# Kernel optimization log

Measured on AMD Instinct MI355X. Metric: run time of the kernel, lower is better.

Reference implementation:

```python
import jax, jax.numpy as jnp
import numpy as np

jax.config.update("jax_enable_x64", True)  # FixedPointMul math is done in float64, as in torch

B, S, H = 8, 4096, 768


def setup_inputs():
    key = jax.random.key(0)
    k = jax.random.split(key, 6)
    s_act = jnp.array([4.0 / 127.0], dtype=jnp.float32)  # per-tensor 8-bit activation scale

    def qact(kk):  # produce int8-quantized-looking activations
        x = jax.random.normal(kk, (B, S, H), jnp.float32)
        return s_act * jnp.clip(jnp.round(x / s_act), -128, 127)

    return {
        "hidden_states": qact(k[0]),
        "hidden_states_scaling_factor": s_act,
        "input_tensor": qact(k[1]),
        "input_tensor_scaling_factor": s_act,
        "dense_weight": 0.02 * jax.random.normal(k[2], (H, H), jnp.float32),
        "dense_bias": 0.01 * jax.random.normal(k[3], (H,), jnp.float32),
        "ln_weight": 1.0 + 0.05 * jax.random.normal(k[4], (H,), jnp.float32),
        "ln_bias": 0.05 * jax.random.normal(k[5], (H,), jnp.float32),
    }


def _sym_scale(k, smin, smax):
    n = 2 ** (k - 1) - 1
    return jnp.clip(jnp.maximum(jnp.abs(smin), jnp.abs(smax)), 1e-8, None) / n


def _sym_quant(x, k, scale):
    n = 2 ** (k - 1) - 1
    return jnp.clip(jnp.round(x / scale), -n, n - 1)


def _batch_frexp(x):
    # returns (round(mantissa * 2^31), 31 - exponent) as in ibert batch_frexp
    m, e = jnp.frexp(x)
    return jnp.floor(m * (2.0 ** 31) + 0.5), 31.0 - e


def _fixedpoint_mul(x, pre_scale, bit, z_scale, identity=None, id_scale=None):
    n = 2 ** (bit - 1) - 1
    ps = jnp.reshape(pre_scale, (1, 1, -1)).astype(jnp.float64)
    z = z_scale.astype(jnp.float64)
    z_int = jnp.round(x.astype(jnp.float64) / ps)
    m, e = _batch_frexp(ps / z)
    out = jnp.round(z_int * m / (2.0 ** e))
    if identity is not None:
        isf = jnp.reshape(id_scale, (1, 1, -1)).astype(jnp.float64)
        wx = jnp.round(identity.astype(jnp.float64) / isf)
        m1, e1 = _batch_frexp(isf / z)
        out = out + jnp.round(wx * m1 / (2.0 ** e1))
    return jnp.clip(out, -n - 1, n).astype(jnp.float32)


def _quant_act(x, bit, pre_scale, identity=None, id_scale=None):
    x_act = x if identity is None else x + identity
    s = _sym_scale(bit, x_act.min(), x_act.max())  # per-tensor scale (dynamic range)
    q = _fixedpoint_mul(x, pre_scale, bit, s, identity, id_scale)
    return q * s, s


def reference(hidden_states, hidden_states_scaling_factor, input_tensor, input_tensor_scaling_factor, dense_weight, dense_bias, ln_weight, ln_bias):
    # ---- QuantLinear: per-channel int8 weights, int32 bias ----
    w_min = dense_weight.min(axis=1)
    w_max = dense_weight.max(axis=1)
    fc_scale = _sym_scale(8, w_min, w_max)                      # [H_out]
    w_int = _sym_quant(dense_weight, 8, fc_scale[:, None])      # [H_out, H_in]
    bias_scale = fc_scale * hidden_states_scaling_factor        # [H_out]
    b_int = _sym_quant(dense_bias, 32, bias_scale)
    x_int = hidden_states / hidden_states_scaling_factor
    hs = (jnp.einsum("bsh,oh->bso", x_int, w_int) + b_int) * bias_scale
    # dropout: eval mode -> identity
    # ---- QuantAct(22-bit) with quantized residual add ----
    hs, ln_in_scale = _quant_act(hs, 22, bias_scale, input_tensor, input_tensor_scaling_factor)
    # ---- IntLayerNorm (integer-only LayerNorm) ----
    x_int = hs / ln_in_scale
    mean_int = jnp.round(jnp.mean(x_int, axis=2, keepdims=True))
    y_int = x_int - mean_int
    var0 = jnp.sum(y_int ** 2, axis=2, keepdims=True)
    shift = jnp.ceil(jnp.log2(jnp.sqrt(jnp.maximum(var0, 1.0) / 2.0 ** 32)))  # set_shift (max_bit=32)
    shift = jnp.maximum(0.0, shift.max())
    y_sh = jnp.floor(y_int / 2.0 ** shift)
    var_int = jnp.sum(y_sh ** 2, axis=2, keepdims=True)
    std_int = jnp.floor(jnp.sqrt(var_int)) * 2.0 ** shift
    factor = jnp.floor(2.0 ** 31 / std_int)
    y_int = jnp.floor(y_int * factor / 2.0)
    sf = jnp.sqrt(jnp.float32(H)) / 2.0 ** 30
    bias_int = jnp.floor((ln_bias / ln_weight) / sf)
    y_int = y_int + bias_int
    sf_out = sf * ln_weight                                     # [H]
    hs = y_int * sf_out
    # ---- QuantAct(8-bit) output requantization ----
    hs, out_scale = _quant_act(hs, 8, sf_out)
    return hs, out_scale
```

## Files before the change

kernel.cpp:

```cpp
#include <hip/hip_runtime.h>

typedef int   v4i   __attribute__((ext_vector_type(4)));
typedef unsigned long u64x2 __attribute__((ext_vector_type(2)));

#define HDIM 768
#define NTOK 32768
#define NCAND 12

static constexpr size_t WX_OFF   = 0;
static constexpr size_t WINT_OFF = 25165824;
static constexpr size_t RS1_OFF  = WINT_OFF + 1179648;
static constexpr size_t RS2_OFF  = RS1_OFF + 6144;
static constexpr size_t BS_OFF   = RS2_OFF + 6144;
static constexpr size_t BINT_OFF = BS_OFF + 3072;
static constexpr size_t LNBI_OFF = BINT_OFF + 3072;
static constexpr size_t SFO_OFF  = LNBI_OFF + 3072;
static constexpr size_t SC_OFF   = SFO_OFF + 3072;
static constexpr size_t RSM1_OFF = SC_OFF + 64;
static constexpr size_t CMIN_OFF = SC_OFF + 128;
static constexpr size_t CMAX_OFF = SC_OFF + 192;
static constexpr size_t FCT_OFF  = SC_OFF + 256;

__device__ __forceinline__ unsigned fenc(float f) {
    unsigned u = __float_as_uint(f);
    return (u >> 31) ? ~u : (u | 0x80000000u);
}
__device__ __forceinline__ float fdec(unsigned e) {
    unsigned u = (e >> 31) ? (e & 0x7fffffffu) : ~e;
    return __uint_as_float(u);
}

#define GLDS16(g, l) __builtin_amdgcn_global_load_lds( \
    (const __attribute__((address_space(1))) unsigned int*)(g), \
    (__attribute__((address_space(3))) unsigned int*)(l), 16, 0, 0)

__device__ __forceinline__ int swz4(int r) { return (r & 3) ^ ((r >> 2) & 3); }

__global__ __launch_bounds__(256) void k0_prep(const float* __restrict__ W,
                                               const float* __restrict__ bias,
                                               const float* __restrict__ ln_w,
                                               const float* __restrict__ ln_b,
                                               const float* __restrict__ phsf,
                                               char* __restrict__ ws) {
    int o = blockIdx.x, tid = threadIdx.x;
    __shared__ float red[256];
    __shared__ float fc_sh;
    float m = 0.f;
    for (int j = tid; j < HDIM; j += 256) m = fmaxf(m, fabsf(W[(size_t)o * HDIM + j]));
    red[tid] = m;
    __syncthreads();
    for (int s = 128; s; s >>= 1) { if (tid < s) red[tid] = fmaxf(red[tid], red[tid + s]); __syncthreads(); }
    if (tid == 0) {
        float fc = fmaxf(red[0], 1e-8f) / 127.0f;
        float hsf = *phsf;
        float bs = fc * hsf;
        fc_sh = fc;
        ((float*)(ws + BS_OFF))[o] = bs;
        ((int*)(ws + BINT_OFF))[o] = (int)rintf(bias[o] / bs);
        float sf = sqrtf(768.0f) / 1073741824.0f;
        float lw = ln_w[o], lb = ln_b[o];
        ((int*)(ws + LNBI_OFF))[o] = (int)floorf((lb / lw) / sf);
        ((float*)(ws + SFO_OFF))[o] = sf * lw;
    }
    __syncthreads();
    float fc = fc_sh;
    char* w8 = (char*)(ws + WINT_OFF);
    for (int j = tid; j < HDIM; j += 256) {
        float q = rintf(W[(size_t)o * HDIM + j] / fc);
        q = fminf(fmaxf(q, -127.f), 126.f);
        w8[(size_t)o * HDIM + j] = (char)q;
    }
    if (blockIdx.x == 0) {
        if (tid < 8) {
            unsigned* sc = (unsigned*)(ws + SC_OFF);
            unsigned v = 0u;
            if (tid == 0 || tid == 2) v = 0xFFFFFFFFu;
            sc[tid] = v;
        }
        if (tid < 16) {
            ((unsigned*)(ws + CMIN_OFF))[tid] = 0xFFFFFFFFu;
            ((unsigned*)(ws + CMAX_OFF))[tid] = 0u;
        }
    }
}

__global__ __launch_bounds__(256) void kp_a8(const float* __restrict__ hs,
                                             const float* __restrict__ phsf,
                                             char* __restrict__ ws) {
    int tid = threadIdx.x;
    size_t b4 = (size_t)blockIdx.x * 1024 + tid;
    float inv = 1.0f / *phsf;
    const float4* in4 = (const float4*)hs;
    unsigned* o32 = (unsigned*)(ws + WX_OFF);
    #pragma unroll
    for (int j = 0; j < 4; ++j) {
        float4 v = in4[b4 + j * 256];
        int q0 = (int)rintf(v.x * inv), q1 = (int)rintf(v.y * inv);
        int q2 = (int)rintf(v.z * inv), q3 = (int)rintf(v.w * inv);
        o32[b4 + j * 256] = (unsigned)(q0 & 255) | ((unsigned)(q1 & 255) << 8) |
                            ((unsigned)(q2 & 255) << 16) | ((unsigned)(q3 & 255) << 24);
    }
}

#define BM 128
#define BN 128
#define BK 64
#define NKT (HDIM / BK)
#define SROW 132
__global__ __launch_bounds__(256, 3) void k1_gemm(const float* __restrict__ inp,
                                                  char* __restrict__ ws,
                                                  int* __restrict__ accOut) {
    __shared__ alignas(16) char smem[32800];
    char* As0 = smem;
    char* Bs0 = smem + 16384;
    float* rmn = (float*)(smem + 32768);
    float* rmx = rmn + 4;
    int tid = threadIdx.x, lane = tid & 63, wave = tid >> 6;
    int wrow = lane & 15, g = lane >> 4;
    int bid = blockIdx.x;
    int xcd = bid & 7, slot = bid >> 3;
    int mtile = xcd * 32 + slot / 6;
    int ntile = slot % 6;
    int t0 = mtile * BM, o0 = ntile * BN;
    const char* a8 = (const char*)(ws + WX_OFF);
    const char* w8 = (const char*)(ws + WINT_OFF);

    const char* asrc[2]; const char* bsrc[2];
    int ldso[2];
    #pragma unroll
    for (int i = 0; i < 2; ++i) {
        int c = i * 256 + tid, r = c >> 2, s = c & 3;
        asrc[i] = a8 + (size_t)(t0 + r) * HDIM + (s ^ swz4(r)) * 16;
        bsrc[i] = w8 + (size_t)(o0 + r) * HDIM + (s ^ swz4(r)) * 16;
        ldso[i] = (i * 256 + wave * 64) * 16;
    }

    int wm = wave & 1, wn = wave >> 1;
    int aofs[4], bofs[4];
    #pragma unroll
    for (int mi = 0; mi < 4; ++mi) { int r = wm * 64 + mi * 16 + wrow; aofs[mi] = r * BK + ((g ^ swz4(r)) * 16); }
    #pragma unroll
    for (int nf = 0; nf < 4; ++nf) { int r = wn * 64 + nf * 16 + wrow; bofs[nf] = r * BK + ((g ^ swz4(r)) * 16); }

    #pragma unroll
    for (int i = 0; i < 2; ++i) GLDS16(asrc[i], As0 + ldso[i]);
    #pragma unroll
    for (int i = 0; i < 2; ++i) GLDS16(bsrc[i], Bs0 + ldso[i]);
    #pragma unroll
    for (int i = 0; i < 2; ++i) GLDS16(asrc[i] + BK, As0 + 8192 + ldso[i]);
    #pragma unroll
    for (int i = 0; i < 2; ++i) GLDS16(bsrc[i] + BK, Bs0 + 8192 + ldso[i]);
    asm volatile("s_waitcnt vmcnt(4)" ::: "memory");
    __builtin_amdgcn_s_barrier();

    v4i acc[4][4] = {};
    for (int kt = 0; kt < NKT; ++kt) {
        int cur = kt & 1;
        const char* Ac = As0 + cur * 8192;
        const char* Bc = Bs0 + cur * 8192;
        u64x2 af[4], bf[4];
        #pragma unroll
        for (int mi = 0; mi < 4; ++mi) af[mi] = *(const u64x2*)(Ac + aofs[mi]);
        #pragma unroll
        for (int nf = 0; nf < 4; ++nf) bf[nf] = *(const u64x2*)(Bc + bofs[nf]);
        asm volatile("s_waitcnt lgkmcnt(0)" ::: "memory");
        __builtin_amdgcn_s_barrier();
        if (kt + 2 < NKT) {
            #pragma unroll
            for (int i = 0; i < 2; ++i) GLDS16(asrc[i] + (kt + 2) * BK, As0 + cur * 8192 + ldso[i]);
            #pragma unroll
            for (int i = 0; i < 2; ++i) GLDS16(bsrc[i] + (kt + 2) * BK, Bs0 + cur * 8192 + ldso[i]);
        }
        __builtin_amdgcn_s_setprio(1);
        #pragma unroll
        for (int mi = 0; mi < 4; ++mi)
            #pragma unroll
            for (int nf = 0; nf < 4; ++nf) {
                acc[mi][nf] = __builtin_amdgcn_mfma_i32_16x16x32_i8((long)af[mi][0], (long)bf[nf][0], acc[mi][nf], 0, 0, 0);
                acc[mi][nf] = __builtin_amdgcn_mfma_i32_16x16x32_i8((long)af[mi][1], (long)bf[nf][1], acc[mi][nf], 0, 0, 0);
            }
        __builtin_amdgcn_s_setprio(0);
        if (kt + 2 < NKT) {
            asm volatile("s_waitcnt vmcnt(4)" ::: "memory");
            __builtin_amdgcn_s_barrier();
        } else if (kt + 2 == NKT) {
            asm volatile("s_waitcnt vmcnt(0)" ::: "memory");
            __builtin_amdgcn_s_barrier();
        }
    }

    const float* bscale = (const float*)(ws + BS_OFF);
    const int* bint = (const int*)(ws + BINT_OFF);
    int* sAcc = (int*)smem;
    float lmn = 3.402823466e38f, lmx = -3.402823466e38f;
    #pragma unroll
    for (int mi = 0; mi < 4; ++mi) {
        __syncthreads();
        #pragma unroll
        for (int nf = 0; nf < 4; ++nf)
            #pragma unroll
            for (int r = 0; r < 4; ++r)
                sAcc[(wm * 16 + g * 4 + r) * SROW + wn * 64 + nf * 16 + wrow] = acc[mi][nf][r];
        __syncthreads();
        #pragma unroll
        for (int k = 0; k < 4; ++k) {
            int i4 = tid + k * 256;
            int sr = i4 >> 5, c4 = i4 & 31;
            int t = t0 + (sr >> 4) * 64 + mi * 16 + (sr & 15);
            int col = o0 + c4 * 4;
            int4 a4 = *(const int4*)&sAcc[sr * SROW + c4 * 4];
            int4 b4 = *(const int4*)&bint[col];
            float4 bs4 = *(const float4*)&bscale[col];
            a4.x += b4.x; a4.y += b4.y; a4.z += b4.z; a4.w += b4.w;
            size_t idx = (size_t)t * HDIM + col;
            *(int4*)&accOut[idx] = a4;
            float4 x4 = *(const float4*)&inp[idx];
            float xa;
            xa = (float)a4.x * bs4.x + x4.x; lmn = fminf(lmn, xa); lmx = fmaxf(lmx, xa);
            xa = (float)a4.y * bs4.y + x4.y; lmn = fminf(lmn, xa); lmx = fmaxf(lmx, xa);
            xa = (float)a4.z * bs4.z + x4.z; lmn = fminf(lmn, xa); lmx = fmaxf(lmx, xa);
            xa = (float)a4.w * bs4.w + x4.w; lmn = fminf(lmn, xa); lmx = fmaxf(lmx, xa);
        }
    }
    #pragma unroll
    for (int off = 32; off; off >>= 1) {
        lmn = fminf(lmn, __shfl_down(lmn, off));
        lmx = fmaxf(lmx, __shfl_down(lmx, off));
    }
    __syncthreads();
    if (lane == 0) { rmn[wave] = lmn; rmx[wave] = lmx; }
    __syncthreads();
    if (tid == 0) {
        float mn = fminf(fminf(rmn[0], rmn[1]), fminf(rmn[2], rmn[3]));
        float mx = fmaxf(fmaxf(rmx[0], rmx[1]), fmaxf(rmx[2], rmx[3]));
        volatile unsigned* sc = (volatile unsigned*)(ws + SC_OFF);
        unsigned emn = fenc(mn), emx = fenc(mx);
        if (emn < sc[0]) atomicMin((unsigned*)&sc[0], emn);
        if (emx > sc[1]) atomicMax((unsigned*)&sc[1], emx);
    }
}

__global__ __launch_bounds__(256) void k2_scale1(const float* __restrict__ pisf, char* __restrict__ ws) {
    __shared__ float s_sh;
    unsigned* sc = (unsigned*)(ws + SC_OFF);
    if (threadIdx.x == 0) {
        float mn = fdec(sc[0]), mx = fdec(sc[1]);
        float s = fmaxf(fmaxf(fabsf(mn), fabsf(mx)), 1e-8f) / 2097151.0f;
        ((float*)sc)[5] = s;
        s_sh = s;
        double r = (double)(*pisf) / (double)s;
        int ex; double mant = frexp(r, &ex);
        double m1 = floor(mant * 2147483648.0 + 0.5);
        ((double*)(ws + RSM1_OFF))[0] = m1 * exp2((double)(ex - 31));
    }
    __syncthreads();
    float s = s_sh;
    const float* bs = (const float*)(ws + BS_OFF);
    double* rs1 = (double*)(ws + RS1_OFF);
    for (int o = threadIdx.x; o < HDIM; o += 256) {
        double r = (double)bs[o] / (double)s;
        int ex; double mant = frexp(r, &ex);
        double m = floor(mant * 2147483648.0 + 0.5);
        rs1[o] = m * exp2((double)(ex - 31));
    }
}

__global__ __launch_bounds__(256) void k3f(char* __restrict__ ws, int* __restrict__ buf,
                                           const float* __restrict__ inp,
                                           const float* __restrict__ pisf) {
    int tid = threadIdx.x, lane = tid & 63, wave = tid >> 6;
    int wid = blockIdx.x * 4 + wave;
    const double* rs1 = (const double*)(ws + RS1_OFF);
    double rsm1 = *(const double*)(ws + RSM1_OFF);
    float inv_isf = 1.0f / *pisf;
    const int* lnbi = (const int*)(ws + LNBI_OFF);
    const float* sfo = (const float*)(ws + SFO_OFF);
    unsigned* fct = (unsigned*)(ws + FCT_OFF);
    __shared__ float smn[4][NCAND], smx[4][NCAND];
    double t_rs1[12]; int t_lnbi[12]; float t_sfo[12];
    #pragma unroll
    for (int c = 0; c < 3; ++c) {
        int o0 = (lane + 64 * c) * 4;
        #pragma unroll
        for (int j = 0; j < 4; ++j) {
            t_rs1[c * 4 + j] = rs1[o0 + j];
            t_lnbi[c * 4 + j] = lnbi[o0 + j];
            t_sfo[c * 4 + j] = sfo[o0 + j];
        }
    }
    int localShift = 0;
    float cmn[NCAND], cmx[NCAND];
    #pragma unroll
    for (int s = 0; s < NCAND; ++s) { cmn[s] = 3.402823466e38f; cmx[s] = -3.402823466e38f; }
    int4 aP[3]; float4 xP[3];
    {
        size_t b0 = (size_t)(wid * 4) * HDIM;
        #pragma unroll
        for (int c = 0; c < 3; ++c) {
            aP[c] = ((const int4*)(buf + b0))[lane + 64 * c];
            xP[c] = ((const float4*)(inp + b0))[lane + 64 * c];
        }
    }
    for (int rr = 0; rr < 4; ++rr) {
        int4 aN[3]; float4 xN[3];
        if (rr < 3) {
            size_t nb = (size_t)(wid * 4 + rr + 1) * HDIM;
            #pragma unroll
            for (int c = 0; c < 3; ++c) {
                aN[c] = ((const int4*)(buf + nb))[lane + 64 * c];
                xN[c] = ((const float4*)(inp + nb))[lane + 64 * c];
            }
        }
        size_t base = (size_t)(wid * 4 + rr) * HDIM;
        int q[12];
        int sum = 0;
        #pragma unroll
        for (int c = 0; c < 3; ++c) {
            int av[4] = {aP[c].x, aP[c].y, aP[c].z, aP[c].w};
            float xv[4] = {xP[c].x, xP[c].y, xP[c].z, xP[c].w};
            #pragma unroll
            for (int j = 0; j < 4; ++j) {
                double q1 = rint((double)av[j] * t_rs1[c * 4 + j]);
                int wxj = (int)rintf(xv[j] * inv_isf);
                double qq = q1 + rint((double)wxj * rsm1);
                qq = fmin(fmax(qq, -2097152.0), 2097151.0);
                q[c * 4 + j] = (int)qq;
                sum += q[c * 4 + j];
            }
        }
        #pragma unroll
        for (int off = 32; off; off >>= 1) sum += __shfl_xor(sum, off);
        int mean = (int)rint((double)sum / 768.0);
        long long v0 = 0;
        #pragma unroll
        for (int k = 0; k < 12; ++k) { q[k] -= mean; v0 += (long long)q[k] * (long long)q[k]; }
        #pragma unroll
        for (int off = 32; off; off >>= 1) v0 += __shfl_xor(v0, off);
        #pragma unroll
        for (int c = 0; c < 3; ++c) {
            int4 y = {q[c * 4 + 0], q[c * 4 + 1], q[c * 4 + 2], q[c * 4 + 3]};
            ((int4*)(buf + base))[lane + 64 * c] = y;
        }
        double vd = (double)(v0 < 1 ? 1LL : v0);
        int sr = (int)ceil(0.5 * log2(vd) - 16.0);
        if (sr < 0) sr = 0;
        localShift = max(localShift, sr);
        #pragma unroll
        for (int s = 0; s < NCAND; ++s) {
            if (s >= sr) {
                long long vs;
                if (s == 0) vs = v0;
                else {
                    vs = 0;
                    #pragma unroll
                    for (int k = 0; k < 12; ++k) { int t = q[k] >> s; vs += (long long)t * (long long)t; }
                    #pragma unroll
                    for (int off = 32; off; off >>= 1) vs += __shfl_xor(vs, off);
                }
                double std_int = floor(sqrt((double)vs)) * (double)(1 << s);
                if (std_int < 1.0) std_int = 1.0;
                long long factor = (long long)floor(2147483648.0 / std_int);
                if (lane == 0) fct[(size_t)(wid * 4 + rr) * 16 + s] = (unsigned)factor;
                #pragma unroll
                for (int k = 0; k < 12; ++k) {
                    long long t = ((long long)q[k] * factor) >> 1;
                    int v2 = (int)t + t_lnbi[k];
                    float h = (float)v2 * t_sfo[k];
                    cmn[s] = fminf(cmn[s], h);
                    cmx[s] = fmaxf(cmx[s], h);
                }
            }
        }
        #pragma unroll
        for (int c = 0; c < 3; ++c) { aP[c] = aN[c]; xP[c] = xN[c]; }
    }
    if (lane == 0 && localShift > 0) {
        int* sp = (int*)(ws + SC_OFF) + 4;
        if (localShift > *(volatile int*)sp) atomicMax(sp, localShift);
    }
    #pragma unroll
    for (int s = 0; s < NCAND; ++s) {
        #pragma unroll
        for (int off = 32; off; off >>= 1) {
            cmn[s] = fminf(cmn[s], __shfl_xor(cmn[s], off));
            cmx[s] = fmaxf(cmx[s], __shfl_xor(cmx[s], off));
        }
    }
    if (lane == 0) {
        #pragma unroll
        for (int s = 0; s < NCAND; ++s) { smn[wave][s] = cmn[s]; smx[wave][s] = cmx[s]; }
    }
    __syncthreads();
    if (tid < NCAND) {
        float m = fminf(fminf(smn[0][tid], smn[1][tid]), fminf(smn[2][tid], smn[3][tid]));
        if (m < 3.3e38f) {
            volatile unsigned* cm = (volatile unsigned*)(ws + CMIN_OFF);
            unsigned e = fenc(m);
            if (e < cm[tid]) atomicMin((unsigned*)&cm[tid], e);
        }
    } else if (tid >= 64 && tid < 64 + NCAND) {
        int s = tid - 64;
        float m = fmaxf(fmaxf(smx[0][s], smx[1][s]), fmaxf(smx[2][s], smx[3][s]));
        if (m > -3.3e38f) {
            volatile unsigned* cm = (volatile unsigned*)(ws + CMAX_OFF);
            unsigned e = fenc(m);
            if (e > cm[s]) atomicMax((unsigned*)&cm[s], e);
        }
    }
}

__global__ __launch_bounds__(256) void k5_scale2(char* __restrict__ ws) {
    __shared__ float s_sh;
    if (threadIdx.x == 0) {
        int shift = ((const int*)(ws + SC_OFF))[4];
        float mn = fdec(((const unsigned*)(ws + CMIN_OFF))[shift]);
        float mx = fdec(((const unsigned*)(ws + CMAX_OFF))[shift]);
        float s2 = fmaxf(fmaxf(fabsf(mn), fabsf(mx)), 1e-8f) / 127.0f;
        ((float*)(ws + SC_OFF))[6] = s2;
        s_sh = s2;
    }
    __syncthreads();
    float s2 = s_sh;
    const float* sfo = (const float*)(ws + SFO_OFF);
    double* rs2 = (double*)(ws + RS2_OFF);
    for (int o = threadIdx.x; o < HDIM; o += 256) {
        double r = (double)sfo[o] / (double)s2;
        int ex; double mant = frexp(r, &ex);
        double m = floor(mant * 2147483648.0 + 0.5);
        rs2[o] = m * exp2((double)(ex - 31));
    }
}

__global__ __launch_bounds__(256) void k6_out(char* __restrict__ ws, float* __restrict__ out) {
    int tid = threadIdx.x, lane = tid & 63, wave = tid >> 6;
    int wid = blockIdx.x * 4 + wave;
    const double* rs2 = (const double*)(ws + RS2_OFF);
    const int* lnbi = (const int*)(ws + LNBI_OFF);
    const unsigned* fct = (const unsigned*)(ws + FCT_OFF);
    int shift = ((const int*)(ws + SC_OFF))[4];
    float s2 = ((const float*)(ws + SC_OFF))[6];
    double t_rs2[12]; int t_lnbi[12];
    #pragma unroll
    for (int c = 0; c < 3; ++c) {
        int o0 = (lane + 64 * c) * 4;
        #pragma unroll
        for (int j = 0; j < 4; ++j) { t_rs2[c * 4 + j] = rs2[o0 + j]; t_lnbi[c * 4 + j] = lnbi[o0 + j]; }
    }
    int* buf = (int*)out;
    int4 yP[3];
    {
        size_t b0 = (size_t)(wid * 4) * HDIM;
        #pragma unroll
        for (int c = 0; c < 3; ++c) yP[c] = ((const int4*)(buf + b0))[lane + 64 * c];
    }
    for (int rr = 0; rr < 4; ++rr) {
        int4 yN[3];
        if (rr < 3) {
            size_t nb = (size_t)(wid * 4 + rr + 1) * HDIM;
            #pragma unroll
            for (int c = 0; c < 3; ++c) yN[c] = ((const int4*)(buf + nb))[lane + 64 * c];
        }
        size_t base = (size_t)(wid * 4 + rr) * HDIM;
        long long factor = (long long)fct[(size_t)(wid * 4 + rr) * 16 + shift];
        int yv[12];
        #pragma unroll
        for (int c = 0; c < 3; ++c) {
            yv[c * 4 + 0] = yP[c].x; yv[c * 4 + 1] = yP[c].y; yv[c * 4 + 2] = yP[c].z; yv[c * 4 + 3] = yP[c].w;
        }
        #pragma unroll
        for (int c = 0; c < 3; ++c) {
            float4 r;
            float* rp = &r.x;
            #pragma unroll
            for (int j = 0; j < 4; ++j) {
                int k = c * 4 + j;
                long long t = ((long long)yv[k] * factor) >> 1;
                int v2 = (int)t + t_lnbi[k];
                double q = rint((double)v2 * t_rs2[k]);
                q = fmin(fmax(q, -128.0), 127.0);
                rp[j] = (float)q * s2;
            }
            ((float4*)(out + base))[lane + 64 * c] = r;
        }
        #pragma unroll
        for (int c = 0; c < 3; ++c) yP[c] = yN[c];
    }
    if (wid == 0 && tid == 0) out[(size_t)NTOK * HDIM] = s2;
}

extern "C" void kernel_launch(void* const* d_in, const int* in_sizes, int n_in,
                              void* d_out, int out_size, void* d_ws, size_t ws_size,
                              hipStream_t stream) {
    const float* hs   = (const float*)d_in[0];
    const float* phsf = (const float*)d_in[1];
    const float* inp  = (const float*)d_in[2];
    const float* pisf = (const float*)d_in[3];
    const float* W    = (const float*)d_in[4];
    const float* bias = (const float*)d_in[5];
    const float* ln_w = (const float*)d_in[6];
    const float* ln_b = (const float*)d_in[7];
    char* ws = (char*)d_ws;
    float* out = (float*)d_out;
    int* buf = (int*)d_out;

    k0_prep<<<HDIM, 256, 0, stream>>>(W, bias, ln_w, ln_b, phsf, ws);
    kp_a8<<<NTOK * HDIM / 4096, 256, 0, stream>>>(hs, phsf, ws);
    k1_gemm<<<(NTOK / BM) * (HDIM / BN), 256, 0, stream>>>(inp, ws, buf);
    k2_scale1<<<1, 256, 0, stream>>>(pisf, ws);
    k3f<<<NTOK / 16, 256, 0, stream>>>(ws, buf, inp, pisf);
    k5_scale2<<<1, 256, 0, stream>>>(ws);
    k6_out<<<NTOK / 16, 256, 0, stream>>>(ws, out);
}
```

Baseline: 422.9 us.

## Limit speculative LayerNorm shift candidates to four per row with fallback pass

The fused LayerNorm stage previously computed min/max statistics for every possible global shift from the row's own shift up to 11, to avoid a second pass. It now evaluates only four candidate shifts per row (sr..sr+3), reusing progressively shifted values, and tracks the minimum row shift. A flag kernel detects when the global shift lies outside that window, and a fallback kernel then recomputes the statistics from the stored centered values. This cuts per-row variance reductions and min/max work, at the cost of two extra launches and per-wave global atomics in place of block-level shared-memory aggregation.

```diff
diff --git a/kernel.cpp b/kernel.cpp
--- a/kernel.cpp
+++ b/kernel.cpp
@@ -5,7 +5,6 @@
 
 #define HDIM 768
 #define NTOK 32768
-#define NCAND 12
 
 static constexpr size_t WX_OFF   = 0;
 static constexpr size_t WINT_OFF = 25165824;
@@ -71,15 +70,16 @@
         w8[(size_t)o * HDIM + j] = (char)q;
     }
     if (blockIdx.x == 0) {
-        if (tid < 8) {
+        if (tid < 16) {
             unsigned* sc = (unsigned*)(ws + SC_OFF);
             unsigned v = 0u;
             if (tid == 0 || tid == 2) v = 0xFFFFFFFFu;
+            if (tid == 8) v = 127u;
             sc[tid] = v;
         }
-        if (tid < 16) {
-            ((unsigned*)(ws + CMIN_OFF))[tid] = 0xFFFFFFFFu;
-            ((unsigned*)(ws + CMAX_OFF))[tid] = 0u;
+        if (tid >= 32 && tid < 48) {
+            ((unsigned*)(ws + CMIN_OFF))[tid - 32] = 0xFFFFFFFFu;
+            ((unsigned*)(ws + CMAX_OFF))[tid - 32] = 0u;
         }
     }
 }
@@ -276,7 +276,8 @@
     const int* lnbi = (const int*)(ws + LNBI_OFF);
     const float* sfo = (const float*)(ws + SFO_OFF);
     unsigned* fct = (unsigned*)(ws + FCT_OFF);
-    __shared__ float smn[4][NCAND], smx[4][NCAND];
+    volatile unsigned* cmi = (volatile unsigned*)(ws + CMIN_OFF);
+    volatile unsigned* cma = (volatile unsigned*)(ws + CMAX_OFF);
     double t_rs1[12]; int t_lnbi[12]; float t_sfo[12];
     #pragma unroll
     for (int c = 0; c < 3; ++c) {
@@ -288,10 +289,7 @@
             t_sfo[c * 4 + j] = sfo[o0 + j];
         }
     }
-    int localShift = 0;
-    float cmn[NCAND], cmx[NCAND];
-    #pragma unroll
-    for (int s = 0; s < NCAND; ++s) { cmn[s] = 3.402823466e38f; cmx[s] = -3.402823466e38f; }
+    int locMax = 0, locMin = 127;
     int4 aP[3]; float4 xP[3];
     {
         size_t b0 = (size_t)(wid * 4) * HDIM;
@@ -344,16 +342,22 @@
         double vd = (double)(v0 < 1 ? 1LL : v0);
         int sr = (int)ceil(0.5 * log2(vd) - 16.0);
         if (sr < 0) sr = 0;
-        localShift = max(localShift, sr);
-        #pragma unroll
-        for (int s = 0; s < NCAND; ++s) {
-            if (s >= sr) {
+        if (sr > 11) sr = 11;
+        locMax = max(locMax, sr);
+        locMin = min(locMin, sr);
+        int z[12];
+        #pragma unroll
+        for (int k = 0; k < 12; ++k) z[k] = q[k] >> sr;
+        #pragma unroll
+        for (int d = 0; d < 4; ++d) {
+            int s = sr + d;
+            if (s < 12) {
                 long long vs;
-                if (s == 0) vs = v0;
+                if (d == 0 && sr == 0) vs = v0;
                 else {
                     vs = 0;
                     #pragma unroll
-                    for (int k = 0; k < 12; ++k) { int t = q[k] >> s; vs += (long long)t * (long long)t; }
+                    for (int k = 0; k < 12; ++k) vs += (long long)z[k] * (long long)z[k];
                     #pragma unroll
                     for (int off = 32; off; off >>= 1) vs += __shfl_xor(vs, off);
                 }
@@ -361,50 +365,101 @@
                 if (std_int < 1.0) std_int = 1.0;
                 long long factor = (long long)floor(2147483648.0 / std_int);
                 if (lane == 0) fct[(size_t)(wid * 4 + rr) * 16 + s] = (unsigned)factor;
+                float hmn = 3.402823466e38f, hmx = -3.402823466e38f;
                 #pragma unroll
                 for (int k = 0; k < 12; ++k) {
                     long long t = ((long long)q[k] * factor) >> 1;
                     int v2 = (int)t + t_lnbi[k];
                     float h = (float)v2 * t_sfo[k];
-                    cmn[s] = fminf(cmn[s], h);
-                    cmx[s] = fmaxf(cmx[s], h);
+                    hmn = fminf(hmn, h);
+                    hmx = fmaxf(hmx, h);
+                }
+                #pragma unroll
+                for (int off = 32; off; off >>= 1) {
+                    hmn = fminf(hmn, __shfl_xor(hmn, off));
+                    hmx = fmaxf(hmx, __shfl_xor(hmx, off));
+                }
+                if (lane == 0) {
+                    unsigned e = fenc(hmn);
+                    if (e < cmi[s]) atomicMin((unsigned*)&cmi[s], e);
+                    e = fenc(hmx);
+                    if (e > cma[s]) atomicMax((unsigned*)&cma[s], e);
                 }
             }
+            #pragma unroll
+            for (int k = 0; k < 12; ++k) z[k] >>= 1;
         }
         #pragma unroll
         for (int c = 0; c < 3; ++c) { aP[c] = aN[c]; xP[c] = xN[c]; }
     }
-    if (lane == 0 && localShift > 0) {
-        int* sp = (int*)(ws + SC_OFF) + 4;
-        if (localShift > *(volatile int*)sp) atomicMax(sp, localShift);
-    }
-    #pragma unroll
-    for (int s = 0; s < NCAND; ++s) {
+    if (lane == 0) {
+        int* sc = (int*)(ws + SC_OFF);
+        if (locMax > 0 && locMax > *(volatile int*)(sc + 4)) atomicMax(sc + 4, locMax);
+        if (locMin < *(volatile int*)(sc + 8)) atomicMin(sc + 8, locMin);
+    }
+}
+
+__global__ void k5a_flag(char* __restrict__ ws) {
+    if (threadIdx.x == 0) {
+        int S = ((const int*)(ws + SC_OFF))[4];
+        int smin = ((const int*)(ws + SC_OFF))[8];
+        ((int*)(ws + SC_OFF))[9] = (S - smin > 3) ? 1 : 0;
+    }
+}
+
+__global__ __launch_bounds__(256) void k4_fb(char* __restrict__ ws, const int* __restrict__ buf) {
+    if (*((volatile int*)(ws + SC_OFF) + 9) == 0) return;
+    int tid = threadIdx.x, lane = tid & 63, wave = tid >> 6;
+    int wid = blockIdx.x * 4 + wave;
+    int S = ((const int*)(ws + SC_OFF))[4];
+    const int* lnbi = (const int*)(ws + LNBI_OFF);
+    const float* sfo = (const float*)(ws + SFO_OFF);
+    unsigned* fct = (unsigned*)(ws + FCT_OFF);
+    volatile unsigned* cmi = (volatile unsigned*)(ws + CMIN_OFF);
+    volatile unsigned* cma = (volatile unsigned*)(ws + CMAX_OFF);
+    int t_lnbi[12]; float t_sfo[12];
+    #pragma unroll
+    for (int c = 0; c < 3; ++c) {
+        int o0 = (lane + 64 * c) * 4;
+        #pragma unroll
+        for (int j = 0; j < 4; ++j) { t_lnbi[c * 4 + j] = lnbi[o0 + j]; t_sfo[c * 4 + j] = sfo[o0 + j]; }
+    }
+    for (int rr = 0; rr < 4; ++rr) {
+        size_t base = (size_t)(wid * 4 + rr) * HDIM;
+        int yv[12];
+        #pragma unroll
+        for (int c = 0; c < 3; ++c) {
+            int4 y4 = ((const int4*)(buf + base))[lane + 64 * c];
+            yv[c * 4 + 0] = y4.x; yv[c * 4 + 1] = y4.y; yv[c * 4 + 2] = y4.z; yv[c * 4 + 3] = y4.w;
+        }
+        long long vs = 0;
+        #pragma unroll
+        for (int k = 0; k < 12; ++k) { int zz = yv[k] >> S; vs += (long long)zz * (long long)zz; }
+        #pragma unroll
+        for (int off = 32; off; off >>= 1) vs += __shfl_xor(vs, off);
+        double std_int = floor(sqrt((double)vs)) * (double)(1 << S);
+        if (std_int < 1.0) std_int = 1.0;
+        long long factor = (long long)floor(2147483648.0 / std_int);
+        if (lane == 0) fct[(size_t)(wid * 4 + rr) * 16 + S] = (unsigned)factor;
+        float hmn = 3.402823466e38f, hmx = -3.402823466e38f;
+        #pragma unroll
+        for (int k = 0; k < 12; ++k) {
+            long long t = ((long long)yv[k] * factor) >> 1;
+            int v2 = (int)t + t_lnbi[k];
+            float h = (float)v2 * t_sfo[k];
+            hmn = fminf(hmn, h);
+            hmx = fmaxf(hmx, h);
+        }
         #pragma unroll
         for (int off = 32; off; off >>= 1) {
-            cmn[s] = fminf(cmn[s], __shfl_xor(cmn[s], off));
-            cmx[s] = fmaxf(cmx[s], __shfl_xor(cmx[s], off));
-        }
-    }
-    if (lane == 0) {
-        #pragma unroll
-        for (int s = 0; s < NCAND; ++s) { smn[wave][s] = cmn[s]; smx[wave][s] = cmx[s]; }
-    }
-    __syncthreads();
-    if (tid < NCAND) {
-        float m = fminf(fminf(smn[0][tid], smn[1][tid]), fminf(smn[2][tid], smn[3][tid]));
-        if (m < 3.3e38f) {
-            volatile unsigned* cm = (volatile unsigned*)(ws + CMIN_OFF);
-            unsigned e = fenc(m);
-            if (e < cm[tid]) atomicMin((unsigned*)&cm[tid], e);
-        }
-    } else if (tid >= 64 && tid < 64 + NCAND) {
-        int s = tid - 64;
-        float m = fmaxf(fmaxf(smx[0][s], smx[1][s]), fmaxf(smx[2][s], smx[3][s]));
-        if (m > -3.3e38f) {
-            volatile unsigned* cm = (volatile unsigned*)(ws + CMAX_OFF);
-            unsigned e = fenc(m);
-            if (e > cm[s]) atomicMax((unsigned*)&cm[s], e);
+            hmn = fminf(hmn, __shfl_xor(hmn, off));
+            hmx = fmaxf(hmx, __shfl_xor(hmx, off));
+        }
+        if (lane == 0) {
+            unsigned e = fenc(hmn);
+            if (e < cmi[S]) atomicMin((unsigned*)&cmi[S], e);
+            e = fenc(hmx);
+            if (e > cma[S]) atomicMax((unsigned*)&cma[S], e);
         }
     }
 }
@@ -508,6 +563,8 @@
     k1_gemm<<<(NTOK / BM) * (HDIM / BN), 256, 0, stream>>>(inp, ws, buf);
     k2_scale1<<<1, 256, 0, stream>>>(pisf, ws);
     k3f<<<NTOK / 16, 256, 0, stream>>>(ws, buf, inp, pisf);
+    k5a_flag<<<1, 64, 0, stream>>>(ws);
+    k4_fb<<<NTOK / 16, 256, 0, stream>>>(ws, buf);
     k5_scale2<<<1, 256, 0, stream>>>(ws);
     k6_out<<<NTOK / 16, 256, 0, stream>>>(ws, out);
 }
```

Measured after the change: 574.0 us. +35.7%, slower.
